# Performance work log

Hardware: AMD Instinct MI355X
Metric: run time of the kernel (lower is better)

The kernel has to match this reference:

```python
import jax, jax.numpy as jnp
import numpy as np

B, L = 16384, 32
IN_DIM, TIME_DIM, HIDDEN, HEADS = 128, 64, 256, 4
HEAD_DIM = HIDDEN // HEADS
KV_DIM = IN_DIM + 2 * TIME_DIM
EPS = 1e-5


def setup_inputs() -> dict:
    key = jax.random.key(0)
    ks = jax.random.split(key, 16)
    s = lambda d: 1.0 / np.sqrt(d)
    return {
        "x_u": jax.random.normal(ks[0], (B, IN_DIM), jnp.float32),
        "x_ctx": jax.random.normal(ks[1], (B, L, IN_DIM), jnp.float32),
        "t_ctx": jax.random.uniform(ks[2], (B, L), jnp.float32) * 100.0,
        "freq": jax.random.normal(ks[3], (TIME_DIM,), jnp.float32),
        "phase": jnp.zeros((TIME_DIM,), jnp.float32),
        "Wq": jax.random.normal(ks[4], (IN_DIM, HIDDEN), jnp.float32) * s(IN_DIM),
        "Wk": jax.random.normal(ks[5], (KV_DIM, HIDDEN), jnp.float32) * s(KV_DIM),
        "Wv": jax.random.normal(ks[6], (KV_DIM, HIDDEN), jnp.float32) * s(KV_DIM),
        "Wres": jax.random.normal(ks[7], (IN_DIM, HIDDEN), jnp.float32) * s(IN_DIM),
        "bres": jnp.zeros((HIDDEN,), jnp.float32),
        "W1": jax.random.normal(ks[8], (HIDDEN, HIDDEN), jnp.float32) * s(HIDDEN),
        "b1": jnp.zeros((HIDDEN,), jnp.float32),
        "W2": jax.random.normal(ks[9], (HIDDEN, HIDDEN), jnp.float32) * s(HIDDEN),
        "b2": jnp.zeros((HIDDEN,), jnp.float32),
        "g1": jnp.ones((HIDDEN,), jnp.float32),
        "be1": jnp.zeros((HIDDEN,), jnp.float32),
        "g2": jnp.ones((HIDDEN,), jnp.float32),
        "be2": jnp.zeros((HIDDEN,), jnp.float32),
    }


def _layernorm(x, g, b):
    m = jnp.mean(x, axis=-1, keepdims=True)
    v = jnp.mean((x - m) ** 2, axis=-1, keepdims=True)
    return (x - m) * jax.lax.rsqrt(v + EPS) * g + b


def reference(x_u, x_ctx, t_ctx, freq, phase, Wq, Wk, Wv, Wres, bres,
              W1, b1, W2, b2, g1, be1, g2, be2):
    # --- time encoding: [B, L, 2*TIME_DIM]
    z = jnp.log1p(jnp.maximum(t_ctx, 0.0))[..., None] * freq + phase
    te = jnp.concatenate([jnp.sin(z), jnp.cos(z)], axis=-1)

    # --- single-query multi-head attention over L neighbors
    q = (x_u @ Wq).reshape(B, HEADS, HEAD_DIM)            # [B,H,d]
    kv = jnp.concatenate([x_ctx, te], axis=-1)            # [B,L,KV_DIM]
    k = (kv @ Wk).reshape(B, L, HEADS, HEAD_DIM)          # [B,L,H,d]
    v = (kv @ Wv).reshape(B, L, HEADS, HEAD_DIM)
    att = jnp.einsum('bhd,blhd->bhl', q, k) / np.sqrt(HEAD_DIM)
    att = jax.nn.softmax(att, axis=-1)                    # [B,H,L]
    agg = jnp.einsum('bhl,blhd->bhd', att, v).reshape(B, HIDDEN)

    # --- residual + norms + FFN (dropout is identity in eval)
    z1 = _layernorm(agg + x_u @ Wres + bres, g1, be1)
    ff = jax.nn.relu(z1 @ W1 + b1) @ W2 + b2
    return _layernorm(ff + z1, g2, be2)
```

## Files before the change

### kernel.cpp

```cpp
#include <hip/hip_runtime.h>

typedef unsigned short u16;
typedef unsigned int   u32;

using bf16x8 = __attribute__((ext_vector_type(8))) short;
using f32x4  = __attribute__((ext_vector_type(4))) float;

#define MFMA16(A, B, C) __builtin_amdgcn_mfma_f32_16x16x32_bf16((A), (B), (C), 0, 0, 0)

static __device__ __forceinline__ u16 f2b(float f) {
    u32 u = __builtin_bit_cast(u32, f);
    u32 r = (u + 0x7FFFu + ((u >> 16) & 1u)) >> 16;
    return (u16)r;
}
static __device__ __forceinline__ u16 f2bh(float f) {
    u32 u = __builtin_bit_cast(u32, f) + 0x8000u;
    return (u16)(u >> 16);
}
static __device__ __forceinline__ u32 pk2(float fa, float fb) {
    u32 a = __builtin_bit_cast(u32, fa) + 0x8000u;
    u32 b = __builtin_bit_cast(u32, fb) + 0x8000u;
    return __builtin_amdgcn_perm(b, a, 0x07060302u);
}
static __device__ __forceinline__ bf16x8 cvt8f(f32x4 a, f32x4 b) {
    union { u32 w[4]; bf16x8 v; } r;
    r.w[0] = pk2(a[0], a[1]); r.w[1] = pk2(a[2], a[3]);
    r.w[2] = pk2(b[0], b[1]); r.w[3] = pk2(b[2], b[3]);
    return r.v;
}
static __device__ __forceinline__ bf16x8 cvt8(f32x4 a, f32x4 b) {
    bf16x8 r;
    r[0] = (short)f2b(a[0]); r[1] = (short)f2b(a[1]);
    r[2] = (short)f2b(a[2]); r[3] = (short)f2b(a[3]);
    r[4] = (short)f2b(b[0]); r[5] = (short)f2b(b[1]);
    r[6] = (short)f2b(b[2]); r[7] = (short)f2b(b[3]);
    return r;
}

__global__ __launch_bounds__(256) void k0_prep(
    const float* __restrict__ Wq, const float* __restrict__ Wk,
    const float* __restrict__ Wv, const float* __restrict__ Wres,
    const float* __restrict__ W1, const float* __restrict__ W2,
    u16* __restrict__ WcatT, u16* __restrict__ WresT,
    u16* __restrict__ WvT, u16* __restrict__ W1T, u16* __restrict__ W2T)
{
    int t = blockIdx.x * 256 + threadIdx.x;
    if (t < 131072) {
        int n = t >> 7, i = t & 127;
        int h = n >> 8, c = n & 255;
        const float* wq = Wq + i * 256 + h * 64;
        const float* wk = Wk + c * 256 + h * 64;
        float acc = 0.f;
        #pragma unroll 8
        for (int d = 0; d < 64; ++d) acc += wq[d] * wk[d];
        WcatT[t] = f2b(acc * 0.125f);
    } else if (t < 163840) {
        int o = t - 131072; int n = o >> 7, i = o & 127;
        WresT[o] = f2b(Wres[i * 256 + n]);
    } else if (t < 229376) {
        int o = t - 163840; int n = o >> 8, c = o & 255;
        WvT[o] = f2b(Wv[c * 256 + n]);
    } else if (t < 294912) {
        int o = t - 229376; int n = o >> 8, c = o & 255;
        W1T[o] = f2b(W1[c * 256 + n]);
    } else {
        int o = t - 294912; int n = o >> 8, c = o & 255;
        W2T[o] = f2b(W2[c * 256 + n]);
    }
}

__global__ __launch_bounds__(512, 6) void kf_fused(
    const float* __restrict__ xu, const float* __restrict__ x_ctx,
    const float* __restrict__ t_ctx, const float* __restrict__ freq,
    const float* __restrict__ phase,
    const u16* __restrict__ WcatT, const u16* __restrict__ WvT,
    const u16* __restrict__ WresT, const u16* __restrict__ W1T,
    const u16* __restrict__ W2T,
    const float* __restrict__ bres, const float* __restrict__ b1,
    const float* __restrict__ b2, const float* __restrict__ g1,
    const float* __restrict__ be1, const float* __restrict__ g2,
    const float* __restrict__ be2, float* __restrict__ out)
{
    __shared__ __align__(16) char smem[39552];
    u16  (*kv)[1032]   = reinterpret_cast<u16 (*)[1032]>(smem);
    u16  (*xus)[136]   = reinterpret_cast<u16 (*)[136]>(smem + 33024);
    u16  (*pw)[4][32]  = reinterpret_cast<u16 (*)[4][32]>(smem + 37376);
    float(*red)[16][2] = reinterpret_cast<float (*)[16][2]>(smem + 37376);
    float(*mrstd)[2]   = reinterpret_cast<float (*)[2]>(smem + 39424);
    float(*zbuf)[264]  = reinterpret_cast<float (*)[264]>(smem);
    u16  (*z1b)[264]   = reinterpret_cast<u16 (*)[264]>(smem + 16896);
    u16  (*h1b)[264]   = reinterpret_cast<u16 (*)[264]>(smem + 25344);
    float(*obuf)[264]  = reinterpret_cast<float (*)[264]>(smem + 16896);

    const int b0 = blockIdx.x * 16;
    const int t = threadIdx.x;
    const int lane = t & 63, wave = t >> 6;
    const int quad = lane >> 4, l16 = lane & 15;
    const int fb = quad * 8;
    const f32x4 zz = {0.f, 0.f, 0.f, 0.f};

    if (t < 256) {
        int row = t >> 4, ch = t & 15;
        const float* src = xu + (size_t)(b0 + row) * 128 + ch * 8;
        *(bf16x8*)&xus[row][ch * 8] = cvt8(*(const f32x4*)src, *(const f32x4*)(src + 4));
    }
    __syncthreads();

    #pragma unroll 2
    for (int nt = 0; nt < 8; ++nt) {
        int n0 = wave * 128 + nt * 16;
        f32x4 acc = zz;
        #pragma unroll
        for (int ks = 0; ks < 4; ++ks) {
            bf16x8 afr = *(const bf16x8*)&xus[l16][ks * 32 + fb];
            bf16x8 bfr = *(const bf16x8*)(WcatT + (size_t)(n0 + l16) * 128 + ks * 32 + fb);
            acc = MFMA16(afr, bfr, acc);
        }
        #pragma unroll
        for (int r = 0; r < 4; ++r)
            kv[quad * 4 + r][n0 + l16] = f2b(acc[r]);
    }
    __syncthreads();

    for (int i = 0; i < 2; ++i) {
        const int kvrow = wave * 2 + i;
        const int b = b0 + kvrow;
        float ltv = log1pf(fmaxf(t_ctx[(size_t)b * 32 + (lane & 31)], 0.f));
        const u16* qb = &kv[kvrow][(l16 & 3) * 256];

        f32x4 accA[2];
        #pragma unroll
        for (int ltile = 0; ltile < 2; ++ltile) {
            const float* xrow = x_ctx + ((size_t)b * 32 + ltile * 16 + l16) * 128;
            f32x4 acc = zz;
            #pragma unroll
            for (int ks = 0; ks < 4; ++ks) {
                f32x4 a = *(const f32x4*)(xrow + ks * 32 + fb);
                f32x4 c = *(const f32x4*)(xrow + ks * 32 + fb + 4);
                acc = MFMA16(cvt8f(a, c), *(const bf16x8*)(qb + ks * 32 + fb), acc);
            }
            float lt_l = __shfl(ltv, ltile * 16 + l16);
            #pragma unroll
            for (int hf = 0; hf < 2; ++hf) {
                f32x4 fa = *(const f32x4*)(freq + hf * 32 + fb);
                f32x4 fc = *(const f32x4*)(freq + hf * 32 + fb + 4);
                f32x4 pa = *(const f32x4*)(phase + hf * 32 + fb);
                f32x4 pc = *(const f32x4*)(phase + hf * 32 + fb + 4);
                f32x4 za = fa * lt_l + pa;
                f32x4 zc = fc * lt_l + pc;
                f32x4 sa, sc;
                #pragma unroll
                for (int j = 0; j < 4; ++j) { sa[j] = __sinf(za[j]); sc[j] = __sinf(zc[j]); }
                acc = MFMA16(cvt8f(sa, sc), *(const bf16x8*)(qb + 128 + hf * 32 + fb), acc);
                #pragma unroll
                for (int j = 0; j < 4; ++j) { sa[j] = __cosf(za[j]); sc[j] = __cosf(zc[j]); }
                acc = MFMA16(cvt8f(sa, sc), *(const bf16x8*)(qb + 192 + hf * 32 + fb), acc);
            }
            accA[ltile] = acc;
        }

        float m = accA[0][0];
        #pragma unroll
        for (int r = 1; r < 4; ++r) m = fmaxf(m, accA[0][r]);
        #pragma unroll
        for (int r = 0; r < 4; ++r) m = fmaxf(m, accA[1][r]);
        m = fmaxf(m, __shfl_xor(m, 16));
        m = fmaxf(m, __shfl_xor(m, 32));
        float p[2][4], s = 0.f;
        #pragma unroll
        for (int lt2 = 0; lt2 < 2; ++lt2)
            #pragma unroll
            for (int r = 0; r < 4; ++r) { p[lt2][r] = __expf(accA[lt2][r] - m); s += p[lt2][r]; }
        s += __shfl_xor(s, 16);
        s += __shfl_xor(s, 32);
        float inv = 1.f / s;
        if (l16 < 4) {
            #pragma unroll
            for (int lt2 = 0; lt2 < 2; ++lt2)
                #pragma unroll
                for (int r = 0; r < 4; ++r)
                    pw[wave][l16][lt2 * 16 + quad * 4 + r] = f2bh(p[lt2][r] * inv);
        }

        bf16x8 pfr = *(const bf16x8*)&pw[wave][l16 & 3][fb];

        #pragma unroll
        for (int nt = 0; nt < 8; ++nt) {
            int c = nt * 16 + l16;
            const float* xp = x_ctx + ((size_t)b * 32 + fb) * 128 + c;
            float v0 = xp[0], v1 = xp[128], v2 = xp[256], v3 = xp[384];
            float v4 = xp[512], v5 = xp[640], v6 = xp[768], v7 = xp[896];
            union { u32 w[4]; bf16x8 v; } bu;
            bu.w[0] = pk2(v0, v1); bu.w[1] = pk2(v2, v3);
            bu.w[2] = pk2(v4, v5); bu.w[3] = pk2(v6, v7);
            f32x4 d = MFMA16(pfr, bu.v, zz);
            if (quad == 0) {
                #pragma unroll
                for (int r = 0; r < 4; ++r) kv[kvrow][r * 256 + c] = f2bh(d[r]);
            }
        }
        float ltj[8];
        #pragma unroll
        for (int j = 0; j < 8; ++j) ltj[j] = __shfl(ltv, fb + j);
        #pragma unroll
        for (int pp = 0; pp < 4; ++pp) {
            int f = pp * 16 + l16;
            float fq = freq[f], phf = phase[f];
            union { u32 w[4]; bf16x8 v; } bs, bc;
            #pragma unroll
            for (int j = 0; j < 4; ++j) {
                float za = ltj[2 * j] * fq + phf;
                float zb = ltj[2 * j + 1] * fq + phf;
                bs.w[j] = pk2(__sinf(za), __sinf(zb));
                bc.w[j] = pk2(__cosf(za), __cosf(zb));
            }
            f32x4 ds = MFMA16(pfr, bs.v, zz);
            f32x4 dc = MFMA16(pfr, bc.v, zz);
            if (quad == 0) {
                #pragma unroll
                for (int r = 0; r < 4; ++r) {
                    kv[kvrow][r * 256 + 128 + f] = f2bh(ds[r]);
                    kv[kvrow][r * 256 + 192 + f] = f2bh(dc[r]);
                }
            }
        }
    }
    __syncthreads();

    const int nw = wave * 32;
    const int hd = (wave >> 1) * 256;

    f32x4 acc[2];
    #pragma unroll
    for (int nt = 0; nt < 2; ++nt) acc[nt] = zz;
    #pragma unroll
    for (int ks = 0; ks < 8; ++ks) {
        bf16x8 afr = *(const bf16x8*)&kv[l16][hd + ks * 32 + quad * 8];
        #pragma unroll
        for (int nt = 0; nt < 2; ++nt) {
            bf16x8 bfr = *(const bf16x8*)(WvT + (size_t)(nw + nt * 16 + l16) * 256 + ks * 32 + quad * 8);
            acc[nt] = MFMA16(afr, bfr, acc[nt]);
        }
    }
    #pragma unroll
    for (int ks = 0; ks < 4; ++ks) {
        bf16x8 afr = *(const bf16x8*)&xus[l16][ks * 32 + quad * 8];
        #pragma unroll
        for (int nt = 0; nt < 2; ++nt) {
            bf16x8 bfr = *(const bf16x8*)(WresT + (size_t)(nw + nt * 16 + l16) * 128 + ks * 32 + quad * 8);
            acc[nt] = MFMA16(afr, bfr, acc[nt]);
        }
    }
    __syncthreads();
    #pragma unroll
    for (int nt = 0; nt < 2; ++nt) {
        int col = nw + nt * 16 + l16;
        float bb = bres[col];
        #pragma unroll
        for (int r = 0; r < 4; ++r)
            zbuf[quad * 4 + r][col] = acc[nt][r] + bb;
    }
    __syncthreads();

    if (t < 256) {
        int row = t >> 4, j = t & 15;
        float s = 0.f, s2 = 0.f;
        #pragma unroll
        for (int i2 = 0; i2 < 16; ++i2) { float v = zbuf[row][j + 16 * i2]; s += v; s2 += v * v; }
        red[row][j][0] = s; red[row][j][1] = s2;
    }
    __syncthreads();
    if (t < 16) {
        float s = 0.f, s2 = 0.f;
        #pragma unroll
        for (int j = 0; j < 16; ++j) { s += red[t][j][0]; s2 += red[t][j][1]; }
        float m = s * (1.f / 256.f);
        float var = s2 * (1.f / 256.f) - m * m;
        mrstd[t][0] = m;
        mrstd[t][1] = rsqrtf(var + 1e-5f);
    }
    __syncthreads();
    {
        int col = t & 255, rh = (t >> 8) * 8;
        float g = g1[col], be = be1[col];
        #pragma unroll
        for (int i2 = 0; i2 < 8; ++i2) {
            int row = rh + i2;
            float z = (zbuf[row][col] - mrstd[row][0]) * mrstd[row][1] * g + be;
            zbuf[row][col] = z;
            z1b[row][col] = f2b(z);
        }
    }
    __syncthreads();

    f32x4 acc2[2];
    #pragma unroll
    for (int nt = 0; nt < 2; ++nt) acc2[nt] = zz;
    #pragma unroll
    for (int ks = 0; ks < 8; ++ks) {
        bf16x8 afr = *(const bf16x8*)&z1b[l16][ks * 32 + quad * 8];
        #pragma unroll
        for (int nt = 0; nt < 2; ++nt) {
            bf16x8 bfr = *(const bf16x8*)(W1T + (size_t)(nw + nt * 16 + l16) * 256 + ks * 32 + quad * 8);
            acc2[nt] = MFMA16(afr, bfr, acc2[nt]);
        }
    }
    #pragma unroll
    for (int nt = 0; nt < 2; ++nt) {
        int col = nw + nt * 16 + l16;
        float bb = b1[col];
        #pragma unroll
        for (int r = 0; r < 4; ++r)
            h1b[quad * 4 + r][col] = f2b(fmaxf(acc2[nt][r] + bb, 0.f));
    }
    __syncthreads();

    f32x4 acc3[2];
    #pragma unroll
    for (int nt = 0; nt < 2; ++nt) acc3[nt] = zz;
    #pragma unroll
    for (int ks = 0; ks < 8; ++ks) {
        bf16x8 afr = *(const bf16x8*)&h1b[l16][ks * 32 + quad * 8];
        #pragma unroll
        for (int nt = 0; nt < 2; ++nt) {
            bf16x8 bfr = *(const bf16x8*)(W2T + (size_t)(nw + nt * 16 + l16) * 256 + ks * 32 + quad * 8);
            acc3[nt] = MFMA16(afr, bfr, acc3[nt]);
        }
    }
    __syncthreads();
    #pragma unroll
    for (int nt = 0; nt < 2; ++nt) {
        int col = nw + nt * 16 + l16;
        float bb = b2[col];
        #pragma unroll
        for (int r = 0; r < 4; ++r) {
            int row = quad * 4 + r;
            obuf[row][col] = acc3[nt][r] + bb + zbuf[row][col];
        }
    }
    __syncthreads();

    if (t < 256) {
        int row = t >> 4, j = t & 15;
        float s = 0.f, s2 = 0.f;
        #pragma unroll
        for (int i2 = 0; i2 < 16; ++i2) { float v = obuf[row][j + 16 * i2]; s += v; s2 += v * v; }
        red[row][j][0] = s; red[row][j][1] = s2;
    }
    __syncthreads();
    if (t < 16) {
        float s = 0.f, s2 = 0.f;
        #pragma unroll
        for (int j = 0; j < 16; ++j) { s += red[t][j][0]; s2 += red[t][j][1]; }
        float m = s * (1.f / 256.f);
        float var = s2 * (1.f / 256.f) - m * m;
        mrstd[t][0] = m;
        mrstd[t][1] = rsqrtf(var + 1e-5f);
    }
    __syncthreads();
    {
        int col = t & 255, rh = (t >> 8) * 8;
        float g = g2[col], be = be2[col];
        #pragma unroll
        for (int i2 = 0; i2 < 8; ++i2) {
            int row = rh + i2;
            out[(size_t)(b0 + row) * 256 + col] =
                (obuf[row][col] - mrstd[row][0]) * mrstd[row][1] * g + be;
        }
    }
}

extern "C" void kernel_launch(void* const* d_in, const int* in_sizes, int n_in,
                              void* d_out, int out_size, void* d_ws, size_t ws_size,
                              hipStream_t stream)
{
    (void)in_sizes; (void)n_in; (void)out_size; (void)ws_size;
    const float* xu    = (const float*)d_in[0];
    const float* x_ctx = (const float*)d_in[1];
    const float* t_ctx = (const float*)d_in[2];
    const float* freq  = (const float*)d_in[3];
    const float* phase = (const float*)d_in[4];
    const float* Wq    = (const float*)d_in[5];
    const float* Wk    = (const float*)d_in[6];
    const float* Wv    = (const float*)d_in[7];
    const float* Wres  = (const float*)d_in[8];
    const float* bres  = (const float*)d_in[9];
    const float* W1    = (const float*)d_in[10];
    const float* b1    = (const float*)d_in[11];
    const float* W2    = (const float*)d_in[12];
    const float* b2    = (const float*)d_in[13];
    const float* g1    = (const float*)d_in[14];
    const float* be1   = (const float*)d_in[15];
    const float* g2    = (const float*)d_in[16];
    const float* be2   = (const float*)d_in[17];
    float* out = (float*)d_out;

    char* ws = (char*)d_ws;
    u16* WcatT = (u16*)(ws);
    u16* WresT = (u16*)(ws + 262144);
    u16* WvT   = (u16*)(ws + 327680);
    u16* W1T   = (u16*)(ws + 458752);
    u16* W2T   = (u16*)(ws + 589824);

    hipLaunchKernelGGL(k0_prep, dim3(1408), dim3(256), 0, stream,
                       Wq, Wk, Wv, Wres, W1, W2, WcatT, WresT, WvT, W1T, W2T);
    hipLaunchKernelGGL(kf_fused, dim3(1024), dim3(512), 0, stream,
                       xu, x_ctx, t_ctx, freq, phase,
                       WcatT, WvT, WresT, W1T, W2T,
                       bres, b1, b2, g1, be1, g2, be2, out);
}
```

Measured before the change: 530.8 us.

## Hoist x_ctx loads ahead of compute and interleave sin/cos work to hide latency

All x_ctx row loads for the score MFMAs are issued up front behind a sched_barrier. The time-encoding sin/cos is computed before the MFMA chain, which is split into two independent accumulators. The value-aggregation phase batches strided x_ctx loads per half and overlaps them with the time-encoding MFMAs. The occupancy hint drops from 6 to 4 blocks so the extra live registers fit, and the prep kernel's Wq·Wk dot product is vectorized to float4. The aim is to hide global load latency with independent ALU work, at the cost of fewer resident waves.

```diff
diff --git a/kernel.cpp b/kernel.cpp
--- a/kernel.cpp
+++ b/kernel.cpp
@@ -48,12 +48,12 @@
     if (t < 131072) {
         int n = t >> 7, i = t & 127;
         int h = n >> 8, c = n & 255;
-        const float* wq = Wq + i * 256 + h * 64;
-        const float* wk = Wk + c * 256 + h * 64;
-        float acc = 0.f;
-        #pragma unroll 8
-        for (int d = 0; d < 64; ++d) acc += wq[d] * wk[d];
-        WcatT[t] = f2b(acc * 0.125f);
+        const f32x4* wq = (const f32x4*)(Wq + i * 256 + h * 64);
+        const f32x4* wk = (const f32x4*)(Wk + c * 256 + h * 64);
+        f32x4 a4 = {0.f, 0.f, 0.f, 0.f};
+        #pragma unroll
+        for (int d = 0; d < 16; ++d) a4 += wq[d] * wk[d];
+        WcatT[t] = f2b((a4[0] + a4[1] + a4[2] + a4[3]) * 0.125f);
     } else if (t < 163840) {
         int o = t - 131072; int n = o >> 7, i = o & 127;
         WresT[o] = f2b(Wres[i * 256 + n]);
@@ -69,7 +69,7 @@
     }
 }
 
-__global__ __launch_bounds__(512, 6) void kf_fused(
+__global__ __launch_bounds__(512, 4) void kf_fused(
     const float* __restrict__ xu, const float* __restrict__ x_ctx,
     const float* __restrict__ t_ctx, const float* __restrict__ freq,
     const float* __restrict__ phase,
@@ -128,18 +128,23 @@
         float ltv = log1pf(fmaxf(t_ctx[(size_t)b * 32 + (lane & 31)], 0.f));
         const u16* qb = &kv[kvrow][(l16 & 3) * 256];
 
+        f32x4 xa[2][4], xc[2][4];
+        #pragma unroll
+        for (int lt = 0; lt < 2; ++lt) {
+            const float* xrow = x_ctx + ((size_t)b * 32 + lt * 16 + l16) * 128;
+            #pragma unroll
+            for (int ks = 0; ks < 4; ++ks) {
+                xa[lt][ks] = *(const f32x4*)(xrow + ks * 32 + fb);
+                xc[lt][ks] = *(const f32x4*)(xrow + ks * 32 + fb + 4);
+            }
+        }
+        __builtin_amdgcn_sched_barrier(0);
+
         f32x4 accA[2];
         #pragma unroll
-        for (int ltile = 0; ltile < 2; ++ltile) {
-            const float* xrow = x_ctx + ((size_t)b * 32 + ltile * 16 + l16) * 128;
-            f32x4 acc = zz;
-            #pragma unroll
-            for (int ks = 0; ks < 4; ++ks) {
-                f32x4 a = *(const f32x4*)(xrow + ks * 32 + fb);
-                f32x4 c = *(const f32x4*)(xrow + ks * 32 + fb + 4);
-                acc = MFMA16(cvt8f(a, c), *(const bf16x8*)(qb + ks * 32 + fb), acc);
-            }
-            float lt_l = __shfl(ltv, ltile * 16 + l16);
+        for (int lt = 0; lt < 2; ++lt) {
+            float lt_l = __shfl(ltv, lt * 16 + l16);
+            bf16x8 te_s[2], te_c[2];
             #pragma unroll
             for (int hf = 0; hf < 2; ++hf) {
                 f32x4 fa = *(const f32x4*)(freq + hf * 32 + fb);
@@ -151,12 +156,21 @@
                 f32x4 sa, sc;
                 #pragma unroll
                 for (int j = 0; j < 4; ++j) { sa[j] = __sinf(za[j]); sc[j] = __sinf(zc[j]); }
-                acc = MFMA16(cvt8f(sa, sc), *(const bf16x8*)(qb + 128 + hf * 32 + fb), acc);
+                te_s[hf] = cvt8f(sa, sc);
                 #pragma unroll
                 for (int j = 0; j < 4; ++j) { sa[j] = __cosf(za[j]); sc[j] = __cosf(zc[j]); }
-                acc = MFMA16(cvt8f(sa, sc), *(const bf16x8*)(qb + 192 + hf * 32 + fb), acc);
+                te_c[hf] = cvt8f(sa, sc);
             }
-            accA[ltile] = acc;
+            f32x4 a0 = zz, a1 = zz;
+            a0 = MFMA16(cvt8f(xa[lt][0], xc[lt][0]), *(const bf16x8*)(qb + 0 * 32 + fb), a0);
+            a1 = MFMA16(cvt8f(xa[lt][1], xc[lt][1]), *(const bf16x8*)(qb + 1 * 32 + fb), a1);
+            a0 = MFMA16(cvt8f(xa[lt][2], xc[lt][2]), *(const bf16x8*)(qb + 2 * 32 + fb), a0);
+            a1 = MFMA16(cvt8f(xa[lt][3], xc[lt][3]), *(const bf16x8*)(qb + 3 * 32 + fb), a1);
+            a0 = MFMA16(te_s[0], *(const bf16x8*)(qb + 128 + fb), a0);
+            a1 = MFMA16(te_s[1], *(const bf16x8*)(qb + 160 + fb), a1);
+            a0 = MFMA16(te_c[0], *(const bf16x8*)(qb + 192 + fb), a0);
+            a1 = MFMA16(te_c[1], *(const bf16x8*)(qb + 224 + fb), a1);
+            accA[lt] = a0 + a1;
         }
 
         float m = accA[0][0];
@@ -183,44 +197,52 @@
         }
 
         bf16x8 pfr = *(const bf16x8*)&pw[wave][l16 & 3][fb];
-
-        #pragma unroll
-        for (int nt = 0; nt < 8; ++nt) {
-            int c = nt * 16 + l16;
-            const float* xp = x_ctx + ((size_t)b * 32 + fb) * 128 + c;
-            float v0 = xp[0], v1 = xp[128], v2 = xp[256], v3 = xp[384];
-            float v4 = xp[512], v5 = xp[640], v6 = xp[768], v7 = xp[896];
-            union { u32 w[4]; bf16x8 v; } bu;
-            bu.w[0] = pk2(v0, v1); bu.w[1] = pk2(v2, v3);
-            bu.w[2] = pk2(v4, v5); bu.w[3] = pk2(v6, v7);
-            f32x4 d = MFMA16(pfr, bu.v, zz);
-            if (quad == 0) {
+        float ltj[8];
+        #pragma unroll
+        for (int j = 0; j < 8; ++j) ltj[j] = __shfl(ltv, fb + j);
+
+        #pragma unroll
+        for (int half = 0; half < 2; ++half) {
+            float xv[4][8];
+            #pragma unroll
+            for (int n4 = 0; n4 < 4; ++n4) {
+                const float* xp = x_ctx + ((size_t)b * 32 + fb) * 128 + (half * 4 + n4) * 16 + l16;
                 #pragma unroll
-                for (int r = 0; r < 4; ++r) kv[kvrow][r * 256 + c] = f2bh(d[r]);
+                for (int j = 0; j < 8; ++j) xv[n4][j] = xp[j * 128];
             }
-        }
-        float ltj[8];
-        #pragma unroll
-        for (int j = 0; j < 8; ++j) ltj[j] = __shfl(ltv, fb + j);
-        #pragma unroll
-        for (int pp = 0; pp < 4; ++pp) {
-            int f = pp * 16 + l16;
-            float fq = freq[f], phf = phase[f];
-            union { u32 w[4]; bf16x8 v; } bs, bc;
-            #pragma unroll
-            for (int j = 0; j < 4; ++j) {
-                float za = ltj[2 * j] * fq + phf;
-                float zb = ltj[2 * j + 1] * fq + phf;
-                bs.w[j] = pk2(__sinf(za), __sinf(zb));
-                bc.w[j] = pk2(__cosf(za), __cosf(zb));
+            __builtin_amdgcn_sched_barrier(0);
+            #pragma unroll
+            for (int p2 = 0; p2 < 2; ++p2) {
+                int f = (half * 2 + p2) * 16 + l16;
+                float fq = freq[f], phf = phase[f];
+                union { u32 w[4]; bf16x8 v; } bs, bc;
+                #pragma unroll
+                for (int j = 0; j < 4; ++j) {
+                    float za = ltj[2 * j] * fq + phf;
+                    float zb = ltj[2 * j + 1] * fq + phf;
+                    bs.w[j] = pk2(__sinf(za), __sinf(zb));
+                    bc.w[j] = pk2(__cosf(za), __cosf(zb));
+                }
+                f32x4 ds = MFMA16(pfr, bs.v, zz);
+                f32x4 dc = MFMA16(pfr, bc.v, zz);
+                if (quad == 0) {
+                    #pragma unroll
+                    for (int r = 0; r < 4; ++r) {
+                        kv[kvrow][r * 256 + 128 + f] = f2bh(ds[r]);
+                        kv[kvrow][r * 256 + 192 + f] = f2bh(dc[r]);
+                    }
+                }
             }
-            f32x4 ds = MFMA16(pfr, bs.v, zz);
-            f32x4 dc = MFMA16(pfr, bc.v, zz);
-            if (quad == 0) {
-                #pragma unroll
-                for (int r = 0; r < 4; ++r) {
-                    kv[kvrow][r * 256 + 128 + f] = f2bh(ds[r]);
-                    kv[kvrow][r * 256 + 192 + f] = f2bh(dc[r]);
+            #pragma unroll
+            for (int n4 = 0; n4 < 4; ++n4) {
+                int c = (half * 4 + n4) * 16 + l16;
+                union { u32 w[4]; bf16x8 v; } bu;
+                bu.w[0] = pk2(xv[n4][0], xv[n4][1]); bu.w[1] = pk2(xv[n4][2], xv[n4][3]);
+                bu.w[2] = pk2(xv[n4][4], xv[n4][5]); bu.w[3] = pk2(xv[n4][6], xv[n4][7]);
+                f32x4 d = MFMA16(pfr, bu.v, zz);
+                if (quad == 0) {
+                    #pragma unroll
+                    for (int r = 0; r < 4; ++r) kv[kvrow][r * 256 + c] = f2bh(d[r]);
                 }
             }
         }
```

New measurement: 487.6 us. 1.09x faster.
